# Kernel tuning notes

Measured on AMD Instinct MI355X. Metric: run time of the kernel, lower is better.

## Reference

```python
import jax, jax.numpy as jnp
from jax import lax
import numpy as np

MAX_ITER = 12      # sifting iterations per IMF
TOL = 0.05         # sd tolerance / flatness tolerance
NUM_IMFS = 6       # max IMFs extracted
EPS = 1e-8


def _peak_mask(s):
    # strict local maxima, matching scipy.signal.find_peaks on plateau-free
    # (continuous random) signals: s[i-1] < s[i] > s[i+1]
    interior = (s[:, 1:-1] > s[:, :-2]) & (s[:, 1:-1] > s[:, 2:])
    return jnp.pad(interior, ((0, 0), (1, 1)))  # [B, L] bool


def _interp_env(s, mask):
    # piecewise-linear interpolation through masked peaks, flat extrapolation
    # at the ends (np.interp with left=first peak val, right=last peak val)
    B, L = s.shape
    idx = jnp.arange(L)
    last = lax.cummax(jnp.where(mask, idx, -1), axis=1)               # prev peak idx (-1 if none)
    nxt = lax.cummin(jnp.where(mask, idx, L), axis=1, reverse=True)   # next peak idx (L if none)
    vl = jnp.take_along_axis(s, jnp.clip(last, 0, L - 1), axis=1)
    vr = jnp.take_along_axis(s, jnp.clip(nxt, 0, L - 1), axis=1)
    denom = nxt - last
    frac = jnp.where(denom > 0,
                     (idx - last).astype(s.dtype) / jnp.maximum(denom, 1).astype(s.dtype),
                     jnp.zeros((), s.dtype))
    env = vl + frac * (vr - vl)
    env = jnp.where(last < 0, vr, env)   # left of first peak
    env = jnp.where(nxt >= L, vl, env)   # right of last peak
    return env


def _envelope(s, upper):
    mask = _peak_mask(s) if upper else _peak_mask(-s)
    env = _interp_env(s, mask)
    # fallback when fewer than 2 peaks: running max / running min of s
    fb = lax.cummax(s, axis=1) if upper else lax.cummin(s, axis=1)
    few = mask.sum(axis=1, keepdims=True) < 2
    return jnp.where(few, fb, env)


def _extract_imf(signal):
    # iterative sifting with early-stop masked into a fixed-length scan
    def body(carry, _):
        h, done = carry
        mean = 0.5 * (_envelope(h, True) + _envelope(h, False))
        # sd = sum((h - h_new)^2) / (sum(h^2)+eps) and h - h_new == mean
        sd = jnp.sum(mean ** 2) / (jnp.sum(h ** 2) + EPS)
        conv = sd < TOL
        h_next = jnp.where(done | conv, h, h - mean)
        return (h_next, done | conv), None
    (h, _), _ = lax.scan(body, (signal, jnp.array(False)), None, length=MAX_ITER)
    return h, signal - h


def _emd(x):
    def step(carry, _):
        res, done = carry
        imf, new_res = _extract_imf(res)
        imf = jnp.where(done, jnp.zeros_like(imf), imf)
        new_res = jnp.where(done, res, new_res)
        # _is_residual_flat: var(diff) < tol * var(residual) (torch.var unbiased)
        d = jnp.diff(new_res, axis=-1)
        flat = jnp.var(d, ddof=1) < TOL * jnp.var(new_res, ddof=1)
        return (new_res, done | flat), imf
    (res, _), imfs = lax.scan(step, (x, jnp.array(False)), None, length=NUM_IMFS)
    # stack IMFs and residual: [NUM_IMFS+1, B, L]; IMFs after early stop are zeros
    return jnp.concatenate([imfs, res[None]], axis=0)


def setup_inputs() -> dict:
    key = jax.random.key(0)
    x = jax.random.normal(key, (64, 16384), dtype=jnp.float32)
    return {"x": x}


def reference(x):
    return _emd(x)
```

## Files before the change

### kernel.cpp

```cpp
#include <hip/hip_runtime.h>

#define NL 16384
#define NB 64
#define NT 1024
#define NC (NL / NT)
#define NW (NT / 64)
#define N_ITER 12
#define N_IMFS 6

#pragma clang fp contract(off)

#define HSZ (NL + (NL >> 5))
__device__ __forceinline__ int physi(int i) { return i + (i >> 5); }

#define FMAXV 3.402823466e38f

__global__ __launch_bounds__(NT, 4) void emd_main(
    const float* __restrict__ x, float* __restrict__ out,
    unsigned* cnt, double* sdsl, double* flsl) {
  __shared__ float h[HSZ];
  __shared__ float meanb[HSZ];
  __shared__ int wLU[NW], wLL[NW], wNU[NW], wNL[NW];
  __shared__ float wMx[NW], wMn[NW];
  __shared__ unsigned wCT[NW];
  __shared__ int eLU[NW], eLL[NW], eNU[NW], eNL[NW];
  __shared__ float eMx[NW], eMn[NW];
  __shared__ unsigned sTot;
  __shared__ double tA[NW], tB[NW], tC[NW], tD[NW];
  __shared__ int sFlag;

  const int t = threadIdx.x;
  const int lane = t & 63;
  const int wv = t >> 6;
  const int row = blockIdx.x;
  const int base = t * NC;
  const float* xr = x + (size_t)row * NL;
  float* res = out + (size_t)N_IMFS * NB * NL + (size_t)row * NL;

  for (int m = 0; m < NC; m++) {
    int i = m * NT + t;
    float v = xr[i];
    h[physi(i)] = v;
    res[i] = v;
  }
  __syncthreads();

  unsigned ep = 0;
  bool done = false;

  for (int k = 0; k < N_IMFS; k++) {
    float* outk = out + (size_t)k * NB * NL + (size_t)row * NL;
    if (done) {
      for (int m = 0; m < NC; m++) outk[m * NT + t] = 0.0f;
      continue;
    }

    for (int it = 0; it < N_ITER; it++) {
      unsigned mU = 0, mL = 0;
      int lmU = -1, lmL = -1, cU = 0, cL = 0;
      float rmx = -FMAXV, rmn = FMAXV;
      {
        float hm = (base > 0) ? h[physi(base - 1)] : 0.0f;
        float hc = h[physi(base)];
        #pragma unroll
        for (int j = 0; j < NC; j++) {
          int i = base + j;
          float hp = (i + 1 < NL) ? h[physi(i + 1)] : 0.0f;
          bool in = (i > 0) && (i + 1 < NL);
          if (in && hm < hc && hc > hp) { mU |= (1u << j); lmU = i; cU++; }
          if (in && hm > hc && hc < hp) { mL |= (1u << j); lmL = i; cL++; }
          rmx = fmaxf(rmx, hc);
          rmn = fminf(rmn, hc);
          hm = hc; hc = hp;
        }
      }
      int iLU = lmU, iLL = lmL;
      float iMx = rmx, iMn = rmn;
      int iNU = mU ? (base + __ffs(mU) - 1) : NL;
      int iNL = mL ? (base + __ffs(mL) - 1) : NL;
      unsigned ict = ((unsigned)cU << 16) | (unsigned)cL;
      #pragma unroll
      for (int o = 1; o < 64; o <<= 1) {
        int a = __shfl_up(iLU, o, 64);
        int b = __shfl_up(iLL, o, 64);
        float fa = __shfl_up(iMx, o, 64);
        float fb = __shfl_up(iMn, o, 64);
        int c = __shfl_down(iNU, o, 64);
        int d = __shfl_down(iNL, o, 64);
        unsigned cc = __shfl_down(ict, o, 64);
        if (lane >= o) { iLU = max(iLU, a); iLL = max(iLL, b);
                         iMx = fmaxf(iMx, fa); iMn = fminf(iMn, fb); }
        if (lane + o < 64) { iNU = min(iNU, c); iNL = min(iNL, d); ict += cc; }
      }
      if (lane == 63) { wLU[wv] = iLU; wLL[wv] = iLL; wMx[wv] = iMx; wMn[wv] = iMn; }
      if (lane == 0)  { wNU[wv] = iNU; wNL[wv] = iNL; wCT[wv] = ict; }
      __syncthreads();
      if (t == 0) {
        int aLU = -1, aLL = -1; float aMx = -FMAXV, aMn = FMAXV; unsigned tot = 0;
        for (int w = 0; w < NW; w++) {
          eLU[w] = aLU; aLU = max(aLU, wLU[w]);
          eLL[w] = aLL; aLL = max(aLL, wLL[w]);
          eMx[w] = aMx; aMx = fmaxf(aMx, wMx[w]);
          eMn[w] = aMn; aMn = fminf(aMn, wMn[w]);
          tot += wCT[w];
        }
        int aNU = NL, aNL = NL;
        for (int w = NW - 1; w >= 0; w--) {
          eNU[w] = aNU; aNU = min(aNU, wNU[w]);
          eNL[w] = aNL; aNL = min(aNL, wNL[w]);
        }
        sTot = tot;
      }
      __syncthreads();
      unsigned tot = sTot;
      int totU = (int)(tot >> 16), totL = (int)(tot & 0xffffu);
      int pLU = __shfl_up(iLU, 1, 64); if (lane == 0) pLU = -1;
      int pLL = __shfl_up(iLL, 1, 64); if (lane == 0) pLL = -1;
      float pMx = __shfl_up(iMx, 1, 64); if (lane == 0) pMx = -FMAXV;
      float pMn = __shfl_up(iMn, 1, 64); if (lane == 0) pMn = FMAXV;
      int sNUl = __shfl_down(iNU, 1, 64); if (lane == 63) sNUl = NL;
      int sNLl = __shfl_down(iNL, 1, 64); if (lane == 63) sNLl = NL;
      const int clU = max(eLU[wv], pLU), clL = max(eLL[wv], pLL);
      const float crx = fmaxf(eMx[wv], pMx), crn = fminf(eMn[wv], pMn);
      const int cnU = min(eNU[wv], sNUl), cnL = min(eNL[wv], sNLl);

      double pm2 = 0.0, ph2 = 0.0;
      {
        float rx = crx, rn = crn;
        int gA = -0x7fffffff, gB = -0x7fffffff, gC = -0x7fffffff, gD = -0x7fffffff;
        float vl = 0.0f, vr = 0.0f, wl = 0.0f, wr = 0.0f;
        #pragma unroll
        for (int j = 0; j < NC; j++) {
          int i = base + j;
          float hc = h[physi(i)];
          rx = fmaxf(rx, hc);
          rn = fminf(rn, hc);
          unsigned lowm = 0xFFFFFFFFu >> (31 - j);
          unsigned highm = 0xFFFFFFFFu << j;
          unsigned a;
          a = mU & lowm;  int lU  = a ? (base + 31 - __clz(a)) : clU;
          a = mL & lowm;  int lL  = a ? (base + 31 - __clz(a)) : clL;
          a = mU & highm; int nUv = a ? (base + __ffs(a) - 1) : cnU;
          a = mL & highm; int nLv = a ? (base + __ffs(a) - 1) : cnL;
          if (lU != gA)  { gA = lU;  vl = h[physi(lU < 0 ? 0 : lU)]; }
          if (nUv != gB) { gB = nUv; vr = h[physi(nUv >= NL ? NL - 1 : nUv)]; }
          if (lL != gC)  { gC = lL;  wl = h[physi(lL < 0 ? 0 : lL)]; }
          if (nLv != gD) { gD = nLv; wr = h[physi(nLv >= NL ? NL - 1 : nLv)]; }
          int den = nUv - lU;
          float fracU = (float)(i - lU) / (float)(den > 0 ? den : 1);
          float envU = (den > 0) ? __builtin_fmaf(fracU, vr - vl, vl) : vl;
          if (lU < 0) envU = vr;
          if (nUv >= NL) envU = vl;
          if (totU < 2) envU = rx;
          int den2 = nLv - lL;
          float fracL = (float)(i - lL) / (float)(den2 > 0 ? den2 : 1);
          float envL = (den2 > 0) ? __builtin_fmaf(fracL, wr - wl, wl) : wl;
          if (lL < 0) envL = wr;
          if (nLv >= NL) envL = wl;
          if (totL < 2) envL = rn;
          float mn = 0.5f * (envU + envL);
          meanb[physi(i)] = mn;
          pm2 += (double)mn * (double)mn;
          ph2 += (double)hc * (double)hc;
        }
      }
      #pragma unroll
      for (int o = 1; o < 64; o <<= 1) {
        double a = __shfl_down(pm2, o, 64);
        double b = __shfl_down(ph2, o, 64);
        if (lane + o < 64) { pm2 += a; ph2 += b; }
      }
      if (lane == 0) { tA[wv] = pm2; tB[wv] = ph2; }
      ep++;
      __syncthreads();
      if (t == 0) {
        double sA = 0.0, sB = 0.0;
        for (int w = 0; w < NW; w++) { sA += tA[w]; sB += tB[w]; }
        atomicAdd(&sdsl[(k * N_ITER + it) * 2 + 0], sA);
        atomicAdd(&sdsl[(k * N_ITER + it) * 2 + 1], sB);
        __hip_atomic_fetch_add(cnt, 1u, __ATOMIC_ACQ_REL, __HIP_MEMORY_SCOPE_AGENT);
        unsigned tgt = ep * gridDim.x;
        while (__hip_atomic_load(cnt, __ATOMIC_ACQUIRE, __HIP_MEMORY_SCOPE_AGENT) < tgt)
          __builtin_amdgcn_s_sleep(1);
        double m2 = __hip_atomic_load(&sdsl[(k * N_ITER + it) * 2 + 0],
                                      __ATOMIC_RELAXED, __HIP_MEMORY_SCOPE_AGENT);
        double h2 = __hip_atomic_load(&sdsl[(k * N_ITER + it) * 2 + 1],
                                      __ATOMIC_RELAXED, __HIP_MEMORY_SCOPE_AGENT);
        sFlag = (m2 / (h2 + 1e-8) < 0.05) ? 1 : 0;
      }
      __syncthreads();
      if (sFlag) break;
      #pragma unroll
      for (int q = 0; q < NC / 4; q++) {
        int p0 = physi(base + q * 4);
        float4 hv = *(const float4*)&h[p0];
        float4 mv = *(const float4*)&meanb[p0];
        hv.x -= mv.x; hv.y -= mv.y; hv.z -= mv.z; hv.w -= mv.w;
        *(float4*)&h[p0] = hv;
      }
      __syncthreads();
    }

    double s1 = 0.0, s2 = 0.0, s3 = 0.0, s4 = 0.0;
    {
      float rc = res[base] - h[physi(base)];
      #pragma unroll
      for (int j = 0; j < NC; j++) {
        int i = base + j;
        s1 += (double)rc;
        s2 += (double)rc * (double)rc;
        if (i + 1 < NL) {
          float rnx = res[i + 1] - h[physi(i + 1)];
          float d = rnx - rc;
          s3 += (double)d;
          s4 += (double)d * (double)d;
          rc = rnx;
        }
      }
    }
    #pragma unroll
    for (int o = 1; o < 64; o <<= 1) {
      double a = __shfl_down(s1, o, 64);
      double b = __shfl_down(s2, o, 64);
      double c = __shfl_down(s3, o, 64);
      double d = __shfl_down(s4, o, 64);
      if (lane + o < 64) { s1 += a; s2 += b; s3 += c; s4 += d; }
    }
    if (lane == 0) { tA[wv] = s1; tB[wv] = s2; tC[wv] = s3; tD[wv] = s4; }
    __syncthreads();
    if (t == 0) {
      double S1 = 0.0, S2 = 0.0, S3 = 0.0, S4 = 0.0;
      for (int w = 0; w < NW; w++) { S1 += tA[w]; S2 += tB[w]; S3 += tC[w]; S4 += tD[w]; }
      atomicAdd(&flsl[k * 4 + 0], S1);
      atomicAdd(&flsl[k * 4 + 1], S2);
      atomicAdd(&flsl[k * 4 + 2], S3);
      atomicAdd(&flsl[k * 4 + 3], S4);
    }
    #pragma unroll
    for (int q = 0; q < NC / 4; q++) {
      int i0 = base + q * 4;
      int p0 = physi(i0);
      float4 rv = *(const float4*)&res[i0];
      float4 hv = *(const float4*)&h[p0];
      float4 rq = make_float4(rv.x - hv.x, rv.y - hv.y, rv.z - hv.z, rv.w - hv.w);
      *(float4*)&outk[i0] = hv;
      *(float4*)&res[i0] = rq;
      *(float4*)&h[p0] = rq;
    }
    ep++;
    __syncthreads();
    if (t == 0) {
      __hip_atomic_fetch_add(cnt, 1u, __ATOMIC_ACQ_REL, __HIP_MEMORY_SCOPE_AGENT);
      unsigned tgt = ep * gridDim.x;
      while (__hip_atomic_load(cnt, __ATOMIC_ACQUIRE, __HIP_MEMORY_SCOPE_AGENT) < tgt)
        __builtin_amdgcn_s_sleep(1);
      double S1 = __hip_atomic_load(&flsl[k * 4 + 0], __ATOMIC_RELAXED, __HIP_MEMORY_SCOPE_AGENT);
      double S2 = __hip_atomic_load(&flsl[k * 4 + 1], __ATOMIC_RELAXED, __HIP_MEMORY_SCOPE_AGENT);
      double S3 = __hip_atomic_load(&flsl[k * 4 + 2], __ATOMIC_RELAXED, __HIP_MEMORY_SCOPE_AGENT);
      double S4 = __hip_atomic_load(&flsl[k * 4 + 3], __ATOMIC_RELAXED, __HIP_MEMORY_SCOPE_AGENT);
      double nr = (double)NB * (double)NL;
      double nd = (double)NB * (double)(NL - 1);
      double varr = (S2 - S1 * S1 / nr) / (nr - 1.0);
      double vard = (S4 - S3 * S3 / nd) / (nd - 1.0);
      sFlag = (vard < 0.05 * varr) ? 1 : 0;
    }
    __syncthreads();
    done = done || (sFlag != 0);
  }
}

extern "C" void kernel_launch(void* const* d_in, const int* in_sizes, int n_in,
                              void* d_out, int out_size, void* d_ws, size_t ws_size,
                              hipStream_t stream) {
  const float* x = (const float*)d_in[0];
  float* out = (float*)d_out;
  size_t zb = ws_size < 4096 ? ws_size : 4096;
  hipMemsetAsync(d_ws, 0, zb, stream);
  unsigned* cnt = (unsigned*)d_ws;
  double* sdsl = (double*)((char*)d_ws + 256);
  double* flsl = (double*)((char*)d_ws + 256 + (size_t)N_IMFS * N_ITER * 2 * 8);
  hipLaunchKernelGGL(emd_main, dim3(NB), dim3(NT), 0, stream, x, out, cnt, sdsl, flsl);
}
```

Before: 301.0 us.

## Keep per-thread signal chunk in registers and use ballot-based peak neighbor search

Each thread now holds its 16-element slice of h in registers, and the mean is kept in registers as well, which removes the meanb shared buffer and most shared-memory reads in the peak-detection and envelope loops. Cross-lane previous/next peak lookup uses a wave ballot plus one shuffle instead of a 6-value, 6-step shuffle scan. The running max/min scan and its extra barriers run only when a row has fewer than two peaks. Global loads and stores are vectorized to float4. More live registers per thread could hurt occupancy at 1024 threads per block, and the conditional barrier path relies on totU/totL being uniform across the block.

```diff
diff --git a/kernel.cpp b/kernel.cpp
--- a/kernel.cpp
+++ b/kernel.cpp
@@ -19,7 +19,6 @@
     const float* __restrict__ x, float* __restrict__ out,
     unsigned* cnt, double* sdsl, double* flsl) {
   __shared__ float h[HSZ];
-  __shared__ float meanb[HSZ];
   __shared__ int wLU[NW], wLL[NW], wNU[NW], wNL[NW];
   __shared__ float wMx[NW], wMn[NW];
   __shared__ unsigned wCT[NW];
@@ -37,11 +36,16 @@
   const float* xr = x + (size_t)row * NL;
   float* res = out + (size_t)N_IMFS * NB * NL + (size_t)row * NL;
 
-  for (int m = 0; m < NC; m++) {
-    int i = m * NT + t;
-    float v = xr[i];
-    h[physi(i)] = v;
-    res[i] = v;
+  float hr[NC];
+
+  #pragma unroll
+  for (int q = 0; q < NC / 4; q++) {
+    int i0 = base + q * 4;
+    float4 v = *(const float4*)&xr[i0];
+    hr[q * 4 + 0] = v.x; hr[q * 4 + 1] = v.y;
+    hr[q * 4 + 2] = v.z; hr[q * 4 + 3] = v.w;
+    *(float4*)&h[physi(i0)] = v;
+    *(float4*)&res[i0] = v;
   }
   __syncthreads();
 
@@ -51,7 +55,9 @@
   for (int k = 0; k < N_IMFS; k++) {
     float* outk = out + (size_t)k * NB * NL + (size_t)row * NL;
     if (done) {
-      for (int m = 0; m < NC; m++) outk[m * NT + t] = 0.0f;
+      #pragma unroll
+      for (int q = 0; q < NC / 4; q++)
+        *(float4*)&outk[base + q * 4] = make_float4(0.f, 0.f, 0.f, 0.f);
       continue;
     }
 
@@ -61,90 +67,126 @@
       float rmx = -FMAXV, rmn = FMAXV;
       {
         float hm = (base > 0) ? h[physi(base - 1)] : 0.0f;
-        float hc = h[physi(base)];
         #pragma unroll
         for (int j = 0; j < NC; j++) {
           int i = base + j;
-          float hp = (i + 1 < NL) ? h[physi(i + 1)] : 0.0f;
+          float hc = hr[j];
+          float hp = (j + 1 < NC) ? hr[j + 1]
+                                  : ((i + 1 < NL) ? h[physi(i + 1)] : 0.0f);
           bool in = (i > 0) && (i + 1 < NL);
           if (in && hm < hc && hc > hp) { mU |= (1u << j); lmU = i; cU++; }
           if (in && hm > hc && hc < hp) { mL |= (1u << j); lmL = i; cL++; }
           rmx = fmaxf(rmx, hc);
           rmn = fminf(rmn, hc);
-          hm = hc; hc = hp;
-        }
-      }
-      int iLU = lmU, iLL = lmL;
-      float iMx = rmx, iMn = rmn;
-      int iNU = mU ? (base + __ffs(mU) - 1) : NL;
-      int iNL = mL ? (base + __ffs(mL) - 1) : NL;
+          hm = hc;
+        }
+      }
+      int fpU = mU ? (base + __ffs(mU) - 1) : NL;
+      int fpL = mL ? (base + __ffs(mL) - 1) : NL;
+      unsigned long long bUm = __ballot(mU != 0);
+      unsigned long long bLm = __ballot(mL != 0);
+      {
+        int s;
+        s = bUm ? (63 - __clzll((long long)bUm)) : 0;
+        if (lane == s) wLU[wv] = bUm ? lmU : -1;
+        s = bLm ? (63 - __clzll((long long)bLm)) : 0;
+        if (lane == s) wLL[wv] = bLm ? lmL : -1;
+        s = bUm ? (__ffsll(bUm) - 1) : 0;
+        if (lane == s) wNU[wv] = bUm ? fpU : NL;
+        s = bLm ? (__ffsll(bLm) - 1) : 0;
+        if (lane == s) wNL[wv] = bLm ? fpL : NL;
+      }
       unsigned ict = ((unsigned)cU << 16) | (unsigned)cL;
       #pragma unroll
       for (int o = 1; o < 64; o <<= 1) {
-        int a = __shfl_up(iLU, o, 64);
-        int b = __shfl_up(iLL, o, 64);
-        float fa = __shfl_up(iMx, o, 64);
-        float fb = __shfl_up(iMn, o, 64);
-        int c = __shfl_down(iNU, o, 64);
-        int d = __shfl_down(iNL, o, 64);
         unsigned cc = __shfl_down(ict, o, 64);
-        if (lane >= o) { iLU = max(iLU, a); iLL = max(iLL, b);
-                         iMx = fmaxf(iMx, fa); iMn = fminf(iMn, fb); }
-        if (lane + o < 64) { iNU = min(iNU, c); iNL = min(iNL, d); ict += cc; }
-      }
-      if (lane == 63) { wLU[wv] = iLU; wLL[wv] = iLL; wMx[wv] = iMx; wMn[wv] = iMn; }
-      if (lane == 0)  { wNU[wv] = iNU; wNL[wv] = iNL; wCT[wv] = ict; }
+        if (lane + o < 64) ict += cc;
+      }
+      if (lane == 0) wCT[wv] = ict;
       __syncthreads();
       if (t == 0) {
-        int aLU = -1, aLL = -1; float aMx = -FMAXV, aMn = FMAXV; unsigned tot = 0;
+        int aLU = -1, aLL = -1; unsigned tt = 0;
         for (int w = 0; w < NW; w++) {
           eLU[w] = aLU; aLU = max(aLU, wLU[w]);
           eLL[w] = aLL; aLL = max(aLL, wLL[w]);
-          eMx[w] = aMx; aMx = fmaxf(aMx, wMx[w]);
-          eMn[w] = aMn; aMn = fminf(aMn, wMn[w]);
-          tot += wCT[w];
+          tt += wCT[w];
         }
         int aNU = NL, aNL = NL;
         for (int w = NW - 1; w >= 0; w--) {
           eNU[w] = aNU; aNU = min(aNU, wNU[w]);
           eNL[w] = aNL; aNL = min(aNL, wNL[w]);
         }
-        sTot = tot;
-      }
-      __syncthreads();
-      unsigned tot = sTot;
-      int totU = (int)(tot >> 16), totL = (int)(tot & 0xffffu);
-      int pLU = __shfl_up(iLU, 1, 64); if (lane == 0) pLU = -1;
-      int pLL = __shfl_up(iLL, 1, 64); if (lane == 0) pLL = -1;
-      float pMx = __shfl_up(iMx, 1, 64); if (lane == 0) pMx = -FMAXV;
-      float pMn = __shfl_up(iMn, 1, 64); if (lane == 0) pMn = FMAXV;
-      int sNUl = __shfl_down(iNU, 1, 64); if (lane == 63) sNUl = NL;
-      int sNLl = __shfl_down(iNL, 1, 64); if (lane == 63) sNLl = NL;
-      const int clU = max(eLU[wv], pLU), clL = max(eLL[wv], pLL);
-      const float crx = fmaxf(eMx[wv], pMx), crn = fminf(eMn[wv], pMn);
-      const int cnU = min(eNU[wv], sNUl), cnL = min(eNL[wv], sNLl);
-
+        sTot = tt;
+      }
+      __syncthreads();
+      const unsigned tot = sTot;
+      const int totU = (int)(tot >> 16), totL = (int)(tot & 0xffffu);
+
+      unsigned long long belowU = bUm & ((1ull << lane) - 1ull);
+      unsigned long long belowL = bLm & ((1ull << lane) - 1ull);
+      unsigned long long aboveU = (lane == 63) ? 0ull : (bUm & (~0ull << (lane + 1)));
+      unsigned long long aboveL = (lane == 63) ? 0ull : (bLm & (~0ull << (lane + 1)));
+      int slU = belowU ? (63 - __clzll((long long)belowU)) : 0;
+      int slL = belowL ? (63 - __clzll((long long)belowL)) : 0;
+      int snU = aboveU ? (__ffsll(aboveU) - 1) : 0;
+      int snL = aboveL ? (__ffsll(aboveL) - 1) : 0;
+      int gU  = __shfl(lmU, slU, 64);
+      int gL  = __shfl(lmL, slL, 64);
+      int gNU = __shfl(fpU, snU, 64);
+      int gNL = __shfl(fpL, snL, 64);
+      const int clU = belowU ? gU  : eLU[wv];
+      const int clL = belowL ? gL  : eLL[wv];
+      const int cnU = aboveU ? gNU : eNU[wv];
+      const int cnL = aboveL ? gNL : eNL[wv];
+
+      float crx = -FMAXV, crn = FMAXV;
+      if (totU < 2 || totL < 2) {
+        float iMx = rmx, iMn = rmn;
+        #pragma unroll
+        for (int o = 1; o < 64; o <<= 1) {
+          float fa = __shfl_up(iMx, o, 64);
+          float fb = __shfl_up(iMn, o, 64);
+          if (lane >= o) { iMx = fmaxf(iMx, fa); iMn = fminf(iMn, fb); }
+        }
+        if (lane == 63) { wMx[wv] = iMx; wMn[wv] = iMn; }
+        __syncthreads();
+        if (t == 0) {
+          float aMx = -FMAXV, aMn = FMAXV;
+          for (int w = 0; w < NW; w++) {
+            eMx[w] = aMx; aMx = fmaxf(aMx, wMx[w]);
+            eMn[w] = aMn; aMn = fminf(aMn, wMn[w]);
+          }
+        }
+        __syncthreads();
+        float pMx = __shfl_up(iMx, 1, 64); if (lane == 0) pMx = -FMAXV;
+        float pMn = __shfl_up(iMn, 1, 64); if (lane == 0) pMn = FMAXV;
+        crx = fmaxf(eMx[wv], pMx);
+        crn = fminf(eMn[wv], pMn);
+      }
+
+      float mr[NC];
       double pm2 = 0.0, ph2 = 0.0;
       {
         float rx = crx, rn = crn;
-        int gA = -0x7fffffff, gB = -0x7fffffff, gC = -0x7fffffff, gD = -0x7fffffff;
-        float vl = 0.0f, vr = 0.0f, wl = 0.0f, wr = 0.0f;
+        int curLU = clU, curLL = clL;
+        float vl = h[physi(clU < 0 ? 0 : clU)];
+        float wl = h[physi(clL < 0 ? 0 : clL)];
+        int gB = -0x7fffffff, gD = -0x7fffffff;
+        float vr = 0.0f, wr = 0.0f;
         #pragma unroll
         for (int j = 0; j < NC; j++) {
           int i = base + j;
-          float hc = h[physi(i)];
+          float hc = hr[j];
           rx = fmaxf(rx, hc);
           rn = fminf(rn, hc);
-          unsigned lowm = 0xFFFFFFFFu >> (31 - j);
+          if ((mU >> j) & 1u) { curLU = i; vl = hc; }
+          if ((mL >> j) & 1u) { curLL = i; wl = hc; }
+          int lU = curLU, lL = curLL;
           unsigned highm = 0xFFFFFFFFu << j;
           unsigned a;
-          a = mU & lowm;  int lU  = a ? (base + 31 - __clz(a)) : clU;
-          a = mL & lowm;  int lL  = a ? (base + 31 - __clz(a)) : clL;
           a = mU & highm; int nUv = a ? (base + __ffs(a) - 1) : cnU;
           a = mL & highm; int nLv = a ? (base + __ffs(a) - 1) : cnL;
-          if (lU != gA)  { gA = lU;  vl = h[physi(lU < 0 ? 0 : lU)]; }
           if (nUv != gB) { gB = nUv; vr = h[physi(nUv >= NL ? NL - 1 : nUv)]; }
-          if (lL != gC)  { gC = lL;  wl = h[physi(lL < 0 ? 0 : lL)]; }
           if (nLv != gD) { gD = nLv; wr = h[physi(nLv >= NL ? NL - 1 : nLv)]; }
           int den = nUv - lU;
           float fracU = (float)(i - lU) / (float)(den > 0 ? den : 1);
@@ -159,7 +201,7 @@
           if (nLv >= NL) envL = wl;
           if (totL < 2) envL = rn;
           float mn = 0.5f * (envU + envL);
-          meanb[physi(i)] = mn;
+          mr[j] = mn;
           pm2 += (double)mn * (double)mn;
           ph2 += (double)hc * (double)hc;
         }
@@ -191,26 +233,35 @@
       __syncthreads();
       if (sFlag) break;
       #pragma unroll
+      for (int j = 0; j < NC; j++) hr[j] -= mr[j];
+      #pragma unroll
       for (int q = 0; q < NC / 4; q++) {
-        int p0 = physi(base + q * 4);
-        float4 hv = *(const float4*)&h[p0];
-        float4 mv = *(const float4*)&meanb[p0];
-        hv.x -= mv.x; hv.y -= mv.y; hv.z -= mv.z; hv.w -= mv.w;
-        *(float4*)&h[p0] = hv;
-      }
-      __syncthreads();
-    }
-
+        int i0 = base + q * 4;
+        *(float4*)&h[physi(i0)] = make_float4(hr[q * 4 + 0], hr[q * 4 + 1],
+                                              hr[q * 4 + 2], hr[q * 4 + 3]);
+      }
+      __syncthreads();
+    }
+
+    float rv[NC];
+    #pragma unroll
+    for (int q = 0; q < NC / 4; q++) {
+      float4 v = *(const float4*)&res[base + q * 4];
+      rv[q * 4 + 0] = v.x; rv[q * 4 + 1] = v.y;
+      rv[q * 4 + 2] = v.z; rv[q * 4 + 3] = v.w;
+    }
     double s1 = 0.0, s2 = 0.0, s3 = 0.0, s4 = 0.0;
     {
-      float rc = res[base] - h[physi(base)];
+      float rb = 0.0f;
+      if (base + NC < NL) rb = res[base + NC] - h[physi(base + NC)];
+      float rc = rv[0] - hr[0];
       #pragma unroll
       for (int j = 0; j < NC; j++) {
         int i = base + j;
         s1 += (double)rc;
         s2 += (double)rc * (double)rc;
         if (i + 1 < NL) {
-          float rnx = res[i + 1] - h[physi(i + 1)];
+          float rnx = (j + 1 < NC) ? (rv[j + 1] - hr[j + 1]) : rb;
           float d = rnx - rc;
           s3 += (double)d;
           s4 += (double)d * (double)d;
@@ -239,13 +290,15 @@
     #pragma unroll
     for (int q = 0; q < NC / 4; q++) {
       int i0 = base + q * 4;
-      int p0 = physi(i0);
-      float4 rv = *(const float4*)&res[i0];
-      float4 hv = *(const float4*)&h[p0];
-      float4 rq = make_float4(rv.x - hv.x, rv.y - hv.y, rv.z - hv.z, rv.w - hv.w);
+      float4 hv = make_float4(hr[q * 4 + 0], hr[q * 4 + 1],
+                              hr[q * 4 + 2], hr[q * 4 + 3]);
+      float4 rq = make_float4(rv[q * 4 + 0] - hv.x, rv[q * 4 + 1] - hv.y,
+                              rv[q * 4 + 2] - hv.z, rv[q * 4 + 3] - hv.w);
       *(float4*)&outk[i0] = hv;
       *(float4*)&res[i0] = rq;
-      *(float4*)&h[p0] = rq;
+      *(float4*)&h[physi(i0)] = rq;
+      hr[q * 4 + 0] = rq.x; hr[q * 4 + 1] = rq.y;
+      hr[q * 4 + 2] = rq.z; hr[q * 4 + 3] = rq.w;
     }
     ep++;
     __syncthreads();
```

Result: slower. 459.2 us (+52.6%).
